# Optimization experiments

Measured on AMD Instinct MI355X. Metric: run time of the kernel, lower is better.

## Reference

```python
import jax, jax.numpy as jnp
import numpy as np

N = 6144          # active voxels / points
C = 96            # embed_channels
B = 2             # batch size
D = H = W = 32    # sparse spatial shape
K = 16            # PFAS kNN
DEPTH = 4
GRID_OPTS = np.array([[0.1, 0.1, 0.1], [0.4, 0.4, 0.4], [0.2, 0.2, 0.2]], dtype=np.float32)
BN_EPS = 1e-5


def _bn(x, g, b):
    # BatchNorm1d in training mode: batch stats over the point dim, biased var
    m = x.mean(0)
    v = jnp.var(x, axis=0)
    return (x - m) * jax.lax.rsqrt(v + BN_EPS) * g + b


def _seg_sum(x, seg):
    return jax.ops.segment_sum(x, seg, num_segments=N)


def _forward(indices, x, fp_w, fp_b, fp_g, fp_be, att_w1, att_b1, att_w2, att_b2,
             ff_w1, ff_b1, ff_g, ff_be, ff_w2, ff_b2, sa_w1, sa_b1, sa_w2, sa_b2,
             fj_w1, fj_b1, fj_g, fj_be, fj_w2, fj_b2,
             proj_w, proj_g, proj_be, lw_w, lw_g, lw_be, w_w, adp_w,
             fuse_w, fuse_g, fuse_be, conv1_w, bn1_g, bn1_be, conv2_w, bn2_g, bn2_be):
    # ---- CMPFE ----
    p = jax.nn.relu(_bn(x @ fp_w.T + fp_b, fp_g, fp_be))            # [N,9]
    cd, cl, nm = p[:, :3], p[:, 3:6], p[:, 6:9]

    def _att(f, i):
        h = jax.nn.relu(f @ att_w1[i].T + att_b1[i])
        return jax.nn.sigmoid(h @ att_w2[i].T + att_b2[i])

    enh = jnp.concatenate([cd, cl * _att(cl, 0), nm * _att(nm, 1)], axis=1)
    fu = jax.nn.relu(_bn(enh @ ff_w1.T + ff_b1, ff_g, ff_be)) @ ff_w2.T + ff_b2
    sem = jax.nn.sigmoid(jax.nn.relu(fu @ sa_w1.T + sa_b1) @ sa_w2.T + sa_b2)
    feat = fu * sem + x * (1.0 - sem)                               # new x.features

    # ---- PFAS: kNN geometry stats ----
    coord = indices[:, 1:].astype(jnp.float32)                      # [N,3]
    batch = indices[:, 0]
    sq = jnp.sum(coord * coord, axis=1)
    d2 = sq[:, None] + sq[None, :] - 2.0 * (coord @ coord.T)
    dist = jnp.sqrt(jnp.maximum(d2, 1e-12))
    same = batch[None, :] == batch[:, None]
    eye = jnp.eye(N, dtype=bool)
    dist = jnp.where(same & ~eye, dist, jnp.inf)
    neg_nd, idx = jax.lax.top_k(-dist, K)                           # K nearest
    nbr = coord[idx]                                                # [N,K,3]
    cent = nbr - nbr.mean(axis=1, keepdims=True)
    cov = jnp.einsum('nkd,nke->nde', cent, cent) / (K - 1)
    S = jnp.linalg.svd(cov, compute_uv=False)                       # [N,3] descending
    Sn = S / (S.sum(axis=1, keepdims=True) + 1e-6)
    linearity = Sn[:, 0:1] - (Sn[:, 1] + Sn[:, 2])[:, None]
    mean_dist = (-neg_nd).mean(axis=1, keepdims=True)
    density = 1.0 / (mean_dist + 1e-6)
    fl = jax.nn.relu(_bn(feat @ fj_w1.T + fj_b1, fj_g, fj_be)) @ fj_w2.T + fj_b2
    fp_ = jax.nn.softmax(fl, axis=1)
    tower = (density * 2.0 + fp_[:, 0:1]) / 3.0
    backg = (jnp.maximum(1.0 - linearity, 1.0 - density) + fp_[:, 1:2]) / 3.0
    line = (linearity * 2.0 + fp_[:, 2:3]) / 3.0
    go = jnp.asarray(GRID_OPTS)
    lg = go[2] * jnp.array([1.0, 1.0, 5.0], jnp.float32)            # last dim *5
    grid_sizes = tower * go[0] + backg * go[1] + line * lg + 1e-6   # [N,3]

    # ---- representative grids (N > 200 path) ----
    gm = grid_sizes.mean(axis=1)
    order = jnp.argsort(gm)
    reps = [grid_sizes[order[100:200]].mean(0),
            grid_sizes[order[::-1][:100]].mean(0),
            grid_sizes[order[:100]].mean(0)]

    # ---- voxel-grid clustering (torch_geometric voxel_grid + unique inverse) ----
    start = coord.min(axis=0)

    def _cluster(size):
        size = jnp.clip(size, 1e-6, None)
        c = jnp.clip(jnp.floor((coord - start) / size).astype(jnp.int64), 0, 4095)
        mx = c.max(axis=0) + 1
        ids = ((batch.astype(jnp.int64) * mx[0] + c[:, 0]) * mx[1] + c[:, 1]) * mx[2] + c[:, 2]
        _, inv = jnp.unique(ids, return_inverse=True, size=N, fill_value=0)
        return inv.reshape(-1)

    # ---- adaptive multi-branch scatter softmax aggregation ----
    branch_feats = []
    for i in range(DEPTH - 1):
        seg = _cluster(reps[i])
        cnt = jnp.maximum(_seg_sum(jnp.ones((N, 1), feat.dtype), seg), 1.0)
        pw = jax.nn.relu(_bn(feat @ lw_w[i].T, lw_g[i], lw_be[i]))
        pw = pw - (_seg_sum(pw, seg) / cnt)[seg]
        pw = pw @ w_w[i].T
        pw = jnp.exp(pw - pw.max())
        pw = pw / (_seg_sum(pw, seg)[seg] + 1e-6)
        pf = jax.nn.relu(_bn(feat @ proj_w[i].T, proj_g[i], proj_be[i])) * pw
        branch_feats.append(_seg_sum(pf, seg)[seg])
    adp = jax.nn.softmax(feat @ adp_w.T, axis=1)                    # [N,3]
    agg = jnp.einsum('nc,ncd->nd', adp, jnp.stack(branch_feats, 1))
    last = jax.nn.relu(_bn(feat @ proj_w[-1].T, proj_g[-1], proj_be[-1]))
    fused = jax.nn.relu(_bn(jnp.concatenate([last, agg], 1) @ fuse_w.T, fuse_g, fuse_be)) + feat
    res = fused

    # ---- submanifold sparse conv block (dense scatter form; inactive sites zero,
    #      outputs gathered only at active sites == SubMConv3d) ----
    bi, zi, yi, xi = indices[:, 0], indices[:, 1], indices[:, 2], indices[:, 3]

    def _subm(f, w):
        grid = jnp.zeros((B, D, H, W, C), f.dtype).at[bi, zi, yi, xi].set(f)
        o = jax.lax.conv_general_dilated(grid, w, (1, 1, 1), 'SAME',
                                         dimension_numbers=('NDHWC', 'DHWIO', 'NDHWC'))
        return o[bi, zi, yi, xi]

    f1 = jax.nn.relu(_bn(_subm(fused, conv1_w), bn1_g, bn1_be))
    f2 = _bn(_subm(f1, conv2_w), bn2_g, bn2_be)
    return jax.nn.relu(f2 + res)


def setup_inputs() -> dict:
    key = jax.random.key(0)
    ks = iter(jax.random.split(key, 64))

    def rn(*shape, s=0.05):
        return jax.random.normal(next(ks), shape, jnp.float32) * s

    # unique active voxel coordinates
    rng = np.random.default_rng(0)
    flat = rng.choice(B * D * H * W, size=N, replace=False)
    b = flat // (D * H * W)
    r = flat % (D * H * W)
    z = r // (H * W)
    y = (r % (H * W)) // W
    xw = r % W
    indices = jnp.asarray(np.stack([b, z, y, xw], 1).astype(np.int32))
    Ch = C // 2
    return {
        'x': jax.random.normal(next(ks), (N, C), jnp.float32),
        'indices': indices,
        'fp_w': rn(9, C), 'fp_b': rn(9), 'fp_g': jnp.ones(9), 'fp_be': jnp.zeros(9),
        'att_w1': rn(2, 16, 3), 'att_b1': rn(2, 16), 'att_w2': rn(2, 3, 16), 'att_b2': rn(2, 3),
        'ff_w1': rn(C, 9), 'ff_b1': rn(C), 'ff_g': jnp.ones(C), 'ff_be': jnp.zeros(C),
        'ff_w2': rn(C, C), 'ff_b2': rn(C),
        'sa_w1': rn(Ch, C), 'sa_b1': rn(Ch), 'sa_w2': rn(1, Ch), 'sa_b2': rn(1),
        'fj_w1': rn(64, C), 'fj_b1': rn(64), 'fj_g': jnp.ones(64), 'fj_be': jnp.zeros(64),
        'fj_w2': rn(3, 64), 'fj_b2': rn(3),
        'proj_w': rn(DEPTH, C, C), 'proj_g': jnp.ones((DEPTH, C)), 'proj_be': jnp.zeros((DEPTH, C)),
        'lw_w': rn(DEPTH - 1, C, C), 'lw_g': jnp.ones((DEPTH - 1, C)), 'lw_be': jnp.zeros((DEPTH - 1, C)),
        'w_w': rn(DEPTH - 1, C, C),
        'adp_w': rn(DEPTH - 1, C),
        'fuse_w': rn(C, 2 * C), 'fuse_g': jnp.ones(C), 'fuse_be': jnp.zeros(C),
        'conv1_w': rn(3, 3, 3, C, C), 'bn1_g': jnp.ones(C), 'bn1_be': jnp.zeros(C),
        'conv2_w': rn(3, 3, 3, C, C), 'bn2_g': jnp.ones(C), 'bn2_be': jnp.zeros(C),
    }


def reference(x, indices, fp_w, fp_b, fp_g, fp_be, att_w1, att_b1, att_w2, att_b2,
              ff_w1, ff_b1, ff_g, ff_be, ff_w2, ff_b2, sa_w1, sa_b1, sa_w2, sa_b2,
              fj_w1, fj_b1, fj_g, fj_be, fj_w2, fj_b2,
              proj_w, proj_g, proj_be, lw_w, lw_g, lw_be, w_w, adp_w,
              fuse_w, fuse_g, fuse_be, conv1_w, bn1_g, bn1_be, conv2_w, bn2_g, bn2_be):
    return _forward(indices, x, fp_w, fp_b, fp_g, fp_be, att_w1, att_b1, att_w2, att_b2,
                    ff_w1, ff_b1, ff_g, ff_be, ff_w2, ff_b2, sa_w1, sa_b1, sa_w2, sa_b2,
                    fj_w1, fj_b1, fj_g, fj_be, fj_w2, fj_b2,
                    proj_w, proj_g, proj_be, lw_w, lw_g, lw_be, w_w, adp_w,
                    fuse_w, fuse_g, fuse_be, conv1_w, bn1_g, bn1_be, conv2_w, bn2_g, bn2_be)
```

## Files before the change

kernel.cpp:

```cpp
#include <hip/hip_runtime.h>
#include <cstdint>

#define NPTS 6144
#define CH 96
#define NCELEM (NPTS*CH)
#define HTSZ 16384

__device__ __forceinline__ unsigned fenc(float f){
  unsigned u = __float_as_uint(f);
  return (u & 0x80000000u) ? ~u : (u | 0x80000000u);
}
__device__ __forceinline__ float fdec(unsigned u){
  unsigned b = (u & 0x80000000u) ? (u & 0x7FFFFFFFu) : ~u;
  return __uint_as_float(b);
}

__device__ void eig3(double a00,double a01,double a02,double a11,double a12,double a22,
                     double &e0,double &e1,double &e2){
  double p1 = a01*a01 + a02*a02 + a12*a12;
  double q = (a00+a11+a22)/3.0;
  double b00=a00-q, b11=a11-q, b22=a22-q;
  double p2 = b00*b00 + b11*b11 + b22*b22 + 2.0*p1;
  if (p2 <= 1e-300){ e0=e1=e2=q; return; }
  double pp = sqrt(p2/6.0);
  double inv = 1.0/pp;
  double c00=b00*inv, c01=a01*inv, c02=a02*inv, c11=b11*inv, c12=a12*inv, c22=b22*inv;
  double det = c00*(c11*c22-c12*c12) - c01*(c01*c22-c12*c02) + c02*(c01*c12-c11*c02);
  double r = det*0.5;
  r = r < -1.0 ? -1.0 : (r > 1.0 ? 1.0 : r);
  double phi = acos(r)/3.0;
  e0 = q + 2.0*pp*cos(phi);
  e2 = q + 2.0*pp*cos(phi + 2.0943951023931953);
  e1 = 3.0*q - e0 - e2;
}

__global__ void k_zero(int* p, long n){
  long i = (long)blockIdx.x*blockDim.x + threadIdx.x;
  long st = (long)gridDim.x*blockDim.x;
  for (; i < n; i += st) p[i] = 0;
}
__global__ void k_init(int* table, int* startmin){
  int i = blockIdx.x*blockDim.x + threadIdx.x;
  if (i < 2*32*32*32) table[i] = -1;
  if (i < 3) startmin[i] = 0x7fffffff;
}
__global__ void k_htinit(unsigned long long* keys, int* vals){
  int i = blockIdx.x*blockDim.x + threadIdx.x;
  if (i < 3*HTSZ){ keys[i] = ~0ull; vals[i] = 0x7fffffff; }
}
__global__ void k_pack_min(const int* __restrict__ ind, unsigned* __restrict__ packed, int* startmin){
  __shared__ int mn[3];
  if (threadIdx.x < 3) mn[threadIdx.x] = 0x7fffffff;
  __syncthreads();
  int p = blockIdx.x*blockDim.x + threadIdx.x;
  if (p < NPTS){
    int b = ind[p*4], z = ind[p*4+1], y = ind[p*4+2], x = ind[p*4+3];
    packed[p] = (unsigned)((b<<15)|(z<<10)|(y<<5)|x);
    atomicMin(&mn[0], z); atomicMin(&mn[1], y); atomicMin(&mn[2], x);
  }
  __syncthreads();
  if (threadIdx.x < 3) atomicMin(&startmin[threadIdx.x], mn[threadIdx.x]);
}

__global__ void __launch_bounds__(256) k_mm(
    const float* __restrict__ Abase, const float* __restrict__ Wbase,
    const float* __restrict__ biasBase, float* __restrict__ Obase,
    int CIN, int COUT,
    long sA, long sW, long sO, long sBias,
    const float* __restrict__ statsBase, long sStats,
    const float* __restrict__ gBase, const float* __restrict__ beBase, long sGB,
    const float* __restrict__ SsumBase, const int* __restrict__ segBase, const int* __restrict__ cntBase,
    unsigned* maxenc, int mode)
{
  int zb = blockIdx.y;
  const float* A = Abase + (long)zb*sA;
  const float* W = Wbase + (long)zb*sW;
  float* O = Obase + (long)zb*sO;
  const float* st = statsBase ? statsBase + (long)zb*sStats : nullptr;
  const float* g  = gBase ? gBase + (long)zb*sGB : nullptr;
  const float* be = beBase ? beBase + (long)zb*sGB : nullptr;
  const float* Ss = SsumBase ? SsumBase + (long)zb*NCELEM : nullptr;
  const int* seg  = segBase ? segBase + (long)zb*NPTS : nullptr;
  const int* cnt  = cntBase ? cntBase + (long)zb*NPTS : nullptr;

  __shared__ float Al[32*97];
  __shared__ float Wl[96*97];
  int tid = threadIdx.x;
  int r0 = blockIdx.x*32;
  for (int idx = tid; idx < CIN*COUT; idx += 256){
    int co = idx / CIN, k = idx - co*CIN;
    Wl[k*97 + co] = W[idx];
  }
  for (int idx = tid; idx < 32*CIN; idx += 256){
    int ir = idx / CIN, k = idx - ir*CIN;
    int row = r0 + ir;
    float v = A[(long)row*CIN + k];
    if (mode >= 1) v = fmaxf((v - st[k*2])*st[k*2+1]*g[k] + be[k], 0.f);
    if (mode == 2){
      int s = seg[row];
      float cf = fmaxf((float)cnt[s], 1.f);
      v -= Ss[(long)s*CH + k] / cf;
    }
    Al[ir*97 + k] = v;
  }
  __syncthreads();
  float lmax = -3.4e38f;
  if (COUT == 96){
    int rp = tid >> 4, cg = tid & 15;
    int co0 = cg*6;
    float acc0[6], acc1[6];
    #pragma unroll
    for (int j=0;j<6;++j){
      float b = biasBase ? biasBase[(long)zb*sBias + co0 + j] : 0.f;
      acc0[j] = b; acc1[j] = b;
    }
    int ra = 2*rp, rb = ra+1;
    for (int k=0;k<CIN;++k){
      float a0 = Al[ra*97+k], a1 = Al[rb*97+k];
      #pragma unroll
      for (int j=0;j<6;++j){
        float w = Wl[k*97+co0+j];
        acc0[j] = fmaf(a0, w, acc0[j]);
        acc1[j] = fmaf(a1, w, acc1[j]);
      }
    }
    #pragma unroll
    for (int j=0;j<6;++j){
      O[(long)(r0+ra)*96 + co0 + j] = acc0[j];
      O[(long)(r0+rb)*96 + co0 + j] = acc1[j];
      lmax = fmaxf(lmax, fmaxf(acc0[j], acc1[j]));
    }
  } else {
    for (int idx = tid; idx < 32*COUT; idx += 256){
      int ir = idx/COUT, co = idx - ir*COUT;
      float acc = biasBase ? biasBase[(long)zb*sBias + co] : 0.f;
      for (int k=0;k<CIN;++k) acc = fmaf(Al[ir*97+k], Wl[k*97+co], acc);
      O[(long)(r0+ir)*COUT + co] = acc;
      lmax = fmaxf(lmax, acc);
    }
  }
  if (maxenc){
    __shared__ float rmx[256];
    rmx[tid] = lmax; __syncthreads();
    for (int s2=128; s2>0; s2>>=1){
      if (tid < s2) rmx[tid] = fmaxf(rmx[tid], rmx[tid+s2]);
      __syncthreads();
    }
    if (tid == 0) atomicMax(&maxenc[zb], fenc(rmx[0]));
  }
}

__global__ void __launch_bounds__(256) k_mm_fuse(
    const float* __restrict__ tp3, const float* __restrict__ st,
    const float* __restrict__ pg3, const float* __restrict__ pbe3,
    const float* __restrict__ agg, const float* __restrict__ fw, float* __restrict__ tf)
{
  __shared__ float Al[32*193];
  __shared__ float Wl[96*97];
  int tid = threadIdx.x, r0 = blockIdx.x*32;
  for (int idx = tid; idx < 32*192; idx += 256){
    int ir = idx/192, k = idx - ir*192;
    int row = r0 + ir;
    float v;
    if (k < 96){
      v = tp3[(long)row*96 + k];
      v = fmaxf((v - st[k*2])*st[k*2+1]*pg3[k] + pbe3[k], 0.f);
    } else {
      v = agg[(long)row*96 + (k-96)];
    }
    Al[ir*193 + k] = v;
  }
  int rp = tid >> 4, cg = tid & 15, co0 = cg*6;
  float acc0[6] = {0,0,0,0,0,0}, acc1[6] = {0,0,0,0,0,0};
  int ra = 2*rp, rb = ra+1;
  for (int h=0; h<2; ++h){
    __syncthreads();
    for (int idx = tid; idx < 96*96; idx += 256){
      int co = idx/96, k = idx - co*96;
      Wl[k*97+co] = fw[(long)co*192 + h*96 + k];
    }
    __syncthreads();
    for (int k=0;k<96;++k){
      float a0 = Al[ra*193 + h*96 + k], a1 = Al[rb*193 + h*96 + k];
      #pragma unroll
      for (int j=0;j<6;++j){
        float w = Wl[k*97+co0+j];
        acc0[j] = fmaf(a0, w, acc0[j]);
        acc1[j] = fmaf(a1, w, acc1[j]);
      }
    }
  }
  #pragma unroll
  for (int j=0;j<6;++j){
    tf[(long)(r0+ra)*96 + co0 + j] = acc0[j];
    tf[(long)(r0+rb)*96 + co0 + j] = acc1[j];
  }
}

__global__ void k_stats(const float* __restrict__ Abase, long sA, int COLS,
                        float* __restrict__ statsBase, long sStats){
  int col = blockIdx.x, zb = blockIdx.y;
  const float* A = Abase + (long)zb*sA;
  double s = 0.0, q = 0.0;
  for (int r = threadIdx.x; r < NPTS; r += 256){
    double v = (double)A[(long)r*COLS + col];
    s += v; q += v*v;
  }
  __shared__ double ls[256], lq[256];
  ls[threadIdx.x] = s; lq[threadIdx.x] = q; __syncthreads();
  for (int t=128; t>0; t>>=1){
    if (threadIdx.x < t){ ls[threadIdx.x] += ls[threadIdx.x+t]; lq[threadIdx.x] += lq[threadIdx.x+t]; }
    __syncthreads();
  }
  if (threadIdx.x == 0){
    double mean = ls[0]/NPTS;
    double var = lq[0]/NPTS - mean*mean;
    float* stp = statsBase + (long)zb*sStats + col*2;
    stp[0] = (float)mean;
    stp[1] = (float)(1.0/sqrt(var + 1e-5));
  }
}

__global__ void k_p_att_enh(const float* __restrict__ t9, const float* __restrict__ st,
                            const float* __restrict__ fg, const float* __restrict__ fbe,
                            const float* __restrict__ aw1, const float* __restrict__ ab1,
                            const float* __restrict__ aw2, const float* __restrict__ ab2,
                            float* __restrict__ enh){
  int p = blockIdx.x*blockDim.x + threadIdx.x;
  if (p >= NPTS) return;
  float pp[9];
  #pragma unroll
  for (int c=0;c<9;++c){
    float v = t9[p*9+c];
    pp[c] = fmaxf((v - st[c*2])*st[c*2+1]*fg[c] + fbe[c], 0.f);
  }
  float eo[9];
  eo[0]=pp[0]; eo[1]=pp[1]; eo[2]=pp[2];
  #pragma unroll
  for (int i=0;i<2;++i){
    const float* w1 = aw1 + i*48;
    const float* b1 = ab1 + i*16;
    const float* w2 = aw2 + i*48;
    const float* b2 = ab2 + i*3;
    const float* f = pp + 3 + i*3;
    float h[16];
    #pragma unroll
    for (int j=0;j<16;++j){
      float s = b1[j];
      #pragma unroll
      for (int k=0;k<3;++k) s = fmaf(f[k], w1[j*3+k], s);
      h[j] = fmaxf(s, 0.f);
    }
    #pragma unroll
    for (int o=0;o<3;++o){
      float s = b2[o];
      #pragma unroll
      for (int j=0;j<16;++j) s = fmaf(h[j], w2[o*16+j], s);
      float a = 1.f/(1.f + expf(-s));
      eo[3+i*3+o] = f[o]*a;
    }
  }
  #pragma unroll
  for (int c=0;c<9;++c) enh[p*9+c] = eo[c];
}

__global__ void __launch_bounds__(256) k_sem_feat(
    const float* __restrict__ fu, const float* __restrict__ x,
    const float* __restrict__ w1, const float* __restrict__ b1,
    const float* __restrict__ w2, const float* __restrict__ b2,
    float* __restrict__ feat){
  int wid = (blockIdx.x*blockDim.x + threadIdx.x) >> 6;
  int lane = threadIdx.x & 63;
  if (wid >= NPTS) return;
  const float* fr = fu + (long)wid*96;
  float partial = 0.f;
  if (lane < 48){
    float h = b1[lane];
    for (int k=0;k<96;++k) h = fmaf(fr[k], w1[lane*96+k], h);
    h = fmaxf(h, 0.f);
    partial = h * w2[lane];
  }
  for (int m=32; m; m>>=1) partial += __shfl_xor(partial, m);
  float sem = 1.f/(1.f + expf(-(partial + b2[0])));
  for (int c=lane; c<96; c+=64){
    float f = fr[c];
    feat[(long)wid*96+c] = f*sem + x[(long)wid*96+c]*(1.f - sem);
  }
}

__global__ void __launch_bounds__(256) k_knn(const unsigned* __restrict__ packed,
                                             float* __restrict__ density, float* __restrict__ linearity){
  __shared__ unsigned pk[NPTS];
  for (int i=threadIdx.x; i<NPTS; i+=256) pk[i] = packed[i];
  __syncthreads();
  int pid = blockIdx.x*4 + (threadIdx.x>>6);
  int lane = threadIdx.x & 63;
  unsigned mypc = pk[pid];
  int myb = (int)(mypc>>15);
  int mz = (int)((mypc>>10)&31), my_=(int)((mypc>>5)&31), mx_=(int)(mypc&31);
  const unsigned T = 36u;
  int cnt = 0;
  for (int it=0; it<96; ++it){
    int j = lane + it*64;
    unsigned pc = pk[j];
    int dz = (int)((pc>>10)&31) - mz;
    int dy = (int)((pc>>5)&31) - my_;
    int dx = (int)(pc&31) - mx_;
    unsigned d2 = (unsigned)(dz*dz + dy*dy + dx*dx);
    cnt += (j != pid && (int)(pc>>15) == myb && d2 <= T) ? 1 : 0;
  }
  for (int m=32; m; m>>=1) cnt += __shfl_xor(cnt, m);
  unsigned lim = (cnt >= 16) ? T : 0xFFFFFFFFu;
  unsigned s[16];
  #pragma unroll
  for (int t=0;t<16;++t) s[t] = 0xFFFFFFFFu;
  for (int it=0; it<96; ++it){
    int j = lane + it*64;
    unsigned pc = pk[j];
    if (j != pid && (int)(pc>>15) == myb){
      int dz = (int)((pc>>10)&31) - mz;
      int dy = (int)((pc>>5)&31) - my_;
      int dx = (int)(pc&31) - mx_;
      unsigned d2 = (unsigned)(dz*dz + dy*dy + dx*dx);
      if (d2 <= lim){
        unsigned key = (d2<<13) | (unsigned)j;
        if (key < s[15]){
          s[15] = key;
          #pragma unroll
          for (int t=15;t>0;--t){
            unsigned a = s[t-1], b = s[t];
            unsigned lo = a<b?a:b, hi = a<b?b:a;
            s[t-1]=lo; s[t]=hi;
          }
        }
      }
    }
  }
  float sdist = 0.f;
  int sz=0,sy=0,sx=0,szz=0,syy=0,sxx=0,szy=0,szx=0,syx=0;
  for (int r=0;r<16;++r){
    unsigned m = s[0];
    #pragma unroll
    for (int w=32; w; w>>=1){
      unsigned o = (unsigned)__shfl_xor((int)m, w);
      m = m<o ? m : o;
    }
    bool own = (s[0] == m);
    #pragma unroll
    for (int t=0;t<15;++t) s[t] = own ? s[t+1] : s[t];
    if (own) s[15] = 0xFFFFFFFFu;
    unsigned idx = m & 8191u;
    unsigned d2 = m >> 13;
    sdist += sqrtf((float)d2);
    unsigned pc = pk[idx];
    int nz=(int)((pc>>10)&31), ny=(int)((pc>>5)&31), nx=(int)(pc&31);
    sz+=nz; sy+=ny; sx+=nx;
    szz+=nz*nz; syy+=ny*ny; sxx+=nx*nx; szy+=nz*ny; szx+=nz*nx; syx+=ny*nx;
  }
  if (lane == 0){
    double m0 = sz/16.0, m1 = sy/16.0, m2 = sx/16.0;
    float c00 = (float)(((double)szz - 16.0*m0*m0)/15.0);
    float c11 = (float)(((double)syy - 16.0*m1*m1)/15.0);
    float c22 = (float)(((double)sxx - 16.0*m2*m2)/15.0);
    float c01 = (float)(((double)szy - 16.0*m0*m1)/15.0);
    float c02 = (float)(((double)szx - 16.0*m0*m2)/15.0);
    float c12 = (float)(((double)syx - 16.0*m1*m2)/15.0);
    double e0,e1,e2;
    eig3((double)c00,(double)c01,(double)c02,(double)c11,(double)c12,(double)c22, e0,e1,e2);
    float s0 = (float)fabs(e0), s1 = (float)fabs(e1), s2 = (float)fabs(e2);
    float den = s0 + s1 + s2 + 1e-6f;
    float sn0 = s0/den, sn1 = s1/den, sn2 = s2/den;
    linearity[pid] = sn0 - (sn1 + sn2);
    float md = sdist * (1.f/16.f);
    density[pid] = 1.f/(md + 1e-6f);
  }
}

__global__ void k_geo(const float* __restrict__ t64, const float* __restrict__ st,
                      const float* __restrict__ fg, const float* __restrict__ fbe,
                      const float* __restrict__ w2, const float* __restrict__ b2,
                      const float* __restrict__ density, const float* __restrict__ linearity,
                      float* __restrict__ gsz, float* __restrict__ gm){
  int p = blockIdx.x*blockDim.x + threadIdx.x;
  if (p >= NPTS) return;
  float fl[3];
  #pragma unroll
  for (int o=0;o<3;++o) fl[o] = b2[o];
  for (int k=0;k<64;++k){
    float v = t64[(long)p*64+k];
    v = fmaxf((v - st[k*2])*st[k*2+1]*fg[k] + fbe[k], 0.f);
    #pragma unroll
    for (int o=0;o<3;++o) fl[o] = fmaf(v, w2[o*64+k], fl[o]);
  }
  float mx = fmaxf(fl[0], fmaxf(fl[1], fl[2]));
  float e0 = expf(fl[0]-mx), e1 = expf(fl[1]-mx), e2 = expf(fl[2]-mx);
  float es = e0+e1+e2;
  float p0 = e0/es, p1 = e1/es, p2 = e2/es;
  float den = density[p], lin = linearity[p];
  float tw = (den*2.f + p0)/3.f;
  float bg = (fmaxf(1.f-lin, 1.f-den) + p1)/3.f;
  float ln = (lin*2.f + p2)/3.f;
  float g0 = tw*0.1f + bg*0.4f + ln*0.2f + 1e-6f;
  float g1 = tw*0.1f + bg*0.4f + ln*0.2f + 1e-6f;
  float g2 = tw*0.1f + bg*0.4f + ln*1.0f + 1e-6f;
  gsz[p*3+0]=g0; gsz[p*3+1]=g1; gsz[p*3+2]=g2;
  gm[p] = (g0+g1+g2)/3.f;
}

#define RNKCHUNK 768
__global__ void __launch_bounds__(256) k_rank(const float* __restrict__ gm, int* __restrict__ rank){
  __shared__ unsigned long long lk[RNKCHUNK];
  int j0 = blockIdx.y*RNKCHUNK;
  for (int i=threadIdx.x; i<RNKCHUNK; i+=256){
    int j = j0 + i;
    lk[i] = (((unsigned long long)fenc(gm[j]))<<13) | (unsigned long long)j;
  }
  __syncthreads();
  int p = blockIdx.x*256 + threadIdx.x;
  unsigned long long myk = (((unsigned long long)fenc(gm[p]))<<13) | (unsigned long long)p;
  int cnt = 0;
  #pragma unroll 4
  for (int i=0; i<RNKCHUNK; ++i) cnt += (lk[i] < myk) ? 1 : 0;
  atomicAdd(&rank[p], cnt);
}
__global__ void k_scatter(const int* __restrict__ rank, const float* __restrict__ gsz,
                          float* __restrict__ bkt){
  int p = blockIdx.x*blockDim.x + threadIdx.x;
  if (p >= NPTS) return;
  int r = rank[p];
  int z = -1, t = 0;
  if (r < 100){ z = 2; t = r; }
  else if (r < 200){ z = 0; t = r - 100; }
  else if (r >= NPTS-100){ z = 1; t = r - (NPTS-100); }
  if (z >= 0){
    #pragma unroll
    for (int d=0; d<3; ++d) bkt[(z*100 + t)*3 + d] = gsz[p*3+d];
  }
}
__global__ void k_reps(const float* __restrict__ bkt, float* __restrict__ reps){
  int i = threadIdx.x;
  if (i >= 9) return;
  int z = i/3, d = i - z*3;
  double s = 0.0;
  for (int t=0; t<100; ++t) s += (double)bkt[(z*100 + t)*3 + d];
  reps[i] = (float)(s/100.0);
}

__global__ void k_cluster_c(const int* __restrict__ ind, const float* __restrict__ reps,
                            const int* __restrict__ startmin, int* __restrict__ cbuf, int* mxbuf){
  int z = blockIdx.y;
  int p = blockIdx.x*blockDim.x + threadIdx.x;
  __shared__ int lmx[3];
  if (threadIdx.x < 3) lmx[threadIdx.x] = 0;
  __syncthreads();
  if (p < NPTS){
    #pragma unroll
    for (int d=0; d<3; ++d){
      float sizev = fmaxf(reps[z*3+d], 1e-6f);
      float cf = floorf(((float)ind[p*4+1+d] - (float)startmin[d]) / sizev);
      int ci = (int)cf;
      ci = ci < 0 ? 0 : (ci > 4095 ? 4095 : ci);
      cbuf[((long)z*NPTS + p)*3 + d] = ci;
      atomicMax(&lmx[d], ci);
    }
  }
  __syncthreads();
  if (threadIdx.x < 3) atomicMax(&mxbuf[z*3+threadIdx.x], lmx[threadIdx.x]);
}
__global__ void k_cluster_ids(const int* __restrict__ ind, const int* __restrict__ cbuf,
                              const int* __restrict__ mxbuf, long long* __restrict__ ids){
  int z = blockIdx.y;
  int p = blockIdx.x*blockDim.x + threadIdx.x;
  if (p >= NPTS) return;
  long long mx0 = mxbuf[z*3+0]+1, mx1 = mxbuf[z*3+1]+1, mx2 = mxbuf[z*3+2]+1;
  long long b = ind[p*4];
  const int* cc = cbuf + ((long)z*NPTS + p)*3;
  ids[(long)z*NPTS + p] = ((b*mx0 + cc[0])*mx1 + cc[1])*mx2 + cc[2];
}

__device__ __forceinline__ int ht_hash(unsigned long long id){
  unsigned long long h = id * 0x9E3779B97F4A7C15ull;
  return (int)(h >> 49) & (HTSZ-1);
}
__global__ void k_seg_build(const long long* __restrict__ ids,
                            unsigned long long* __restrict__ keys, int* __restrict__ vals){
  int z = blockIdx.y;
  int p = blockIdx.x*blockDim.x + threadIdx.x;
  if (p >= NPTS) return;
  unsigned long long id = (unsigned long long)ids[(long)z*NPTS + p];
  unsigned long long* K = keys + (long)z*HTSZ;
  int* V = vals + (long)z*HTSZ;
  int slot = ht_hash(id);
  while (true){
    unsigned long long prev = atomicCAS(&K[slot], ~0ull, id);
    if (prev == ~0ull || prev == id){ atomicMin(&V[slot], p); break; }
    slot = (slot + 1) & (HTSZ-1);
  }
}
__global__ void k_seg_lookup(const long long* __restrict__ ids,
                             const unsigned long long* __restrict__ keys, const int* __restrict__ vals,
                             int* __restrict__ seg, int* __restrict__ cnt){
  int z = blockIdx.y;
  int p = blockIdx.x*blockDim.x + threadIdx.x;
  if (p >= NPTS) return;
  unsigned long long id = (unsigned long long)ids[(long)z*NPTS + p];
  const unsigned long long* K = keys + (long)z*HTSZ;
  int slot = ht_hash(id);
  while (K[slot] != id) slot = (slot + 1) & (HTSZ-1);
  int rep = vals[(long)z*HTSZ + slot];
  seg[(long)z*NPTS + p] = rep;
  atomicAdd(&cnt[(long)z*NPTS + rep], 1);
}

__global__ void k_pw_accum(const float* __restrict__ tlw, const float* __restrict__ stats,
                           const float* __restrict__ g, const float* __restrict__ be,
                           const int* __restrict__ seg, float* __restrict__ S){
  int z = blockIdx.y;
  int idx = blockIdx.x*blockDim.x + threadIdx.x;
  int p = idx/CH, c = idx - p*CH;
  const float* st = stats + z*192;
  float v = tlw[(long)z*NCELEM + idx];
  v = fmaxf((v - st[c*2])*st[c*2+1]*g[z*CH+c] + be[z*CH+c], 0.f);
  atomicAdd(&S[(long)z*NCELEM + (long)seg[(long)z*NPTS+p]*CH + c], v);
}
__global__ void k_exp_accum(const float* __restrict__ pw2, const unsigned* __restrict__ maxenc,
                            const int* __restrict__ seg, float* __restrict__ E){
  int z = blockIdx.y;
  int idx = blockIdx.x*blockDim.x + threadIdx.x;
  int p = idx/CH, c = idx - p*CH;
  float mv = fdec(maxenc[z]);
  float v = expf(pw2[(long)z*NCELEM + idx] - mv);
  atomicAdd(&E[(long)z*NCELEM + (long)seg[(long)z*NPTS+p]*CH + c], v);
}
__global__ void k_pf_accum(const float* __restrict__ tp, const float* __restrict__ stats,
                           const float* __restrict__ pg, const float* __restrict__ pbe,
                           const float* __restrict__ pw2, const unsigned* __restrict__ maxenc,
                           const int* __restrict__ seg, const float* __restrict__ E,
                           float* __restrict__ F){
  int z = blockIdx.y;
  int idx = blockIdx.x*blockDim.x + threadIdx.x;
  int p = idx/CH, c = idx - p*CH;
  const float* st = stats + z*192;
  float v = tp[(long)z*NCELEM + idx];
  v = fmaxf((v - st[c*2])*st[c*2+1]*pg[z*CH+c] + pbe[z*CH+c], 0.f);
  float mv = fdec(maxenc[z]);
  int sg = seg[(long)z*NPTS+p];
  float w = expf(pw2[(long)z*NCELEM + idx] - mv) / (E[(long)z*NCELEM + (long)sg*CH + c] + 1e-6f);
  atomicAdd(&F[(long)z*NCELEM + (long)sg*CH + c], v*w);
}
__global__ void k_adp(const float* __restrict__ feat, const float* __restrict__ aw,
                      float* __restrict__ adp){
  int p = blockIdx.x*blockDim.x + threadIdx.x;
  if (p >= NPTS) return;
  float a0=0.f, a1=0.f, a2=0.f;
  for (int k=0;k<CH;++k){
    float f = feat[(long)p*CH+k];
    a0 = fmaf(f, aw[k], a0);
    a1 = fmaf(f, aw[CH+k], a1);
    a2 = fmaf(f, aw[2*CH+k], a2);
  }
  float m = fmaxf(a0, fmaxf(a1,a2));
  float e0 = expf(a0-m), e1 = expf(a1-m), e2 = expf(a2-m);
  float s = e0+e1+e2;
  adp[p*3]=e0/s; adp[p*3+1]=e1/s; adp[p*3+2]=e2/s;
}
__global__ void k_agg(const float* __restrict__ adp, const float* __restrict__ F,
                      const int* __restrict__ seg, float* __restrict__ agg){
  int idx = blockIdx.x*blockDim.x + threadIdx.x;
  int p = idx/CH, c = idx - p*CH;
  float s = 0.f;
  #pragma unroll
  for (int z=0;z<3;++z)
    s = fmaf(adp[p*3+z], F[(long)z*NCELEM + (long)seg[(long)z*NPTS+p]*CH + c], s);
  agg[idx] = s;
}

__global__ void k_fused(const float* __restrict__ tf, const float* __restrict__ st,
                        const float* __restrict__ fg, const float* __restrict__ fbe,
                        const float* __restrict__ feat, float* __restrict__ fused){
  int idx = blockIdx.x*blockDim.x + threadIdx.x;
  int c = idx % CH;
  float v = tf[idx];
  v = fmaxf((v - st[c*2])*st[c*2+1]*fg[c] + fbe[c], 0.f);
  fused[idx] = v + feat[idx];
}
__global__ void k_table(const int* __restrict__ ind, int* __restrict__ table){
  int p = blockIdx.x*blockDim.x + threadIdx.x;
  if (p >= NPTS) return;
  int b = ind[p*4], z = ind[p*4+1], y = ind[p*4+2], x = ind[p*4+3];
  table[((b*32+z)*32+y)*32+x] = p;
}
__global__ void k_nbr(const int* __restrict__ ind, const int* __restrict__ table,
                      int* __restrict__ nbrtab){
  int idx = blockIdx.x*blockDim.x + threadIdx.x;
  if (idx >= NPTS*27) return;
  int p = idx/27, tap = idx - p*27;
  int dz = tap/9 - 1;
  int rm = tap % 9;
  int dy = rm/3 - 1, dx = rm%3 - 1;
  int b = ind[p*4], z = ind[p*4+1]+dz, y = ind[p*4+2]+dy, x = ind[p*4+3]+dx;
  int q = -1;
  if ((unsigned)z < 32u && (unsigned)y < 32u && (unsigned)x < 32u)
    q = table[((b*32+z)*32+y)*32+x];
  nbrtab[idx] = q;
}
__global__ void __launch_bounds__(256) k_convlist(const int* __restrict__ nbrtab,
                                                  int* __restrict__ tapcnt,
                                                  int* __restrict__ ptlist){
  __shared__ int lcnt[27], lbase[27], lpos[27];
  int tid = threadIdx.x;
  if (tid < 27){ lcnt[tid] = 0; lpos[tid] = 0; }
  __syncthreads();
  int base = blockIdx.x * 6912;
  for (int i = tid; i < 6912; i += 256){
    int idx = base + i;
    if (nbrtab[idx] >= 0) atomicAdd(&lcnt[idx % 27], 1);
  }
  __syncthreads();
  if (tid < 27) lbase[tid] = atomicAdd(&tapcnt[tid], lcnt[tid]);
  __syncthreads();
  for (int i = tid; i < 6912; i += 256){
    int idx = base + i;
    int q = nbrtab[idx];
    if (q >= 0){
      int tap = idx % 27;
      int p = idx / 27;
      int pos = lbase[tap] + atomicAdd(&lpos[tap], 1);
      ptlist[tap*NPTS + pos] = (p<<16) | q;
    }
  }
}
__global__ void __launch_bounds__(256) k_conv_gemm(
    const float* __restrict__ src, const float* __restrict__ Wc,
    const int* __restrict__ tapcnt, const int* __restrict__ ptlist,
    float* __restrict__ out){
  int tap = blockIdx.y;
  int n = tapcnt[tap];
  int r0 = blockIdx.x*32;
  if (r0 >= n) return;
  __shared__ float Al[32*97];
  __shared__ float Wl[96*97];
  __shared__ int pqs[32];
  int tid = threadIdx.x;
  if (tid < 32){
    int r = r0 + tid;
    pqs[tid] = (r < n) ? ptlist[tap*NPTS + r] : -1;
  }
  __syncthreads();
  for (int idx4 = tid; idx4 < 2304; idx4 += 256){
    int ci = idx4/24, c4 = idx4 - ci*24;
    float4 w = ((const float4*)(Wc + ((long)tap*96 + ci)*96))[c4];
    float* d = &Wl[ci*97 + c4*4];
    d[0]=w.x; d[1]=w.y; d[2]=w.z; d[3]=w.w;
  }
  for (int idx4 = tid; idx4 < 32*24; idx4 += 256){
    int ir = idx4/24, c4 = idx4 - ir*24;
    int pq = pqs[ir];
    float4 s = make_float4(0.f,0.f,0.f,0.f);
    if (pq >= 0){
      int q = pq & 0xFFFF;
      s = ((const float4*)(src + (long)q*CH))[c4];
    }
    float* d = &Al[ir*97 + c4*4];
    d[0]=s.x; d[1]=s.y; d[2]=s.z; d[3]=s.w;
  }
  __syncthreads();
  int rp = tid >> 4, cg = tid & 15;
  int co0 = cg*6;
  int ra = 2*rp, rb = ra+1;
  float acc0[6]={0,0,0,0,0,0}, acc1[6]={0,0,0,0,0,0};
  for (int k=0;k<96;++k){
    float a0 = Al[ra*97+k], a1 = Al[rb*97+k];
    #pragma unroll
    for (int j=0;j<6;++j){
      float w = Wl[k*97+co0+j];
      acc0[j] = fmaf(a0, w, acc0[j]);
      acc1[j] = fmaf(a1, w, acc1[j]);
    }
  }
  int pa = pqs[ra], pb = pqs[rb];
  if (pa >= 0){
    float* o = out + (long)(pa>>16)*CH + co0;
    #pragma unroll
    for (int j=0;j<6;++j) atomicAdd(&o[j], acc0[j]);
  }
  if (pb >= 0){
    float* o = out + (long)(pb>>16)*CH + co0;
    #pragma unroll
    for (int j=0;j<6;++j) atomicAdd(&o[j], acc1[j]);
  }
}
__global__ void k_bnrelu(const float* __restrict__ a, const float* __restrict__ st,
                         const float* __restrict__ g, const float* __restrict__ be,
                         float* __restrict__ o){
  int idx = blockIdx.x*blockDim.x + threadIdx.x;
  int c = idx % CH;
  float v = a[idx];
  o[idx] = fmaxf((v - st[c*2])*st[c*2+1]*g[c] + be[c], 0.f);
}
__global__ void k_final(const float* __restrict__ c2, const float* __restrict__ st,
                        const float* __restrict__ g, const float* __restrict__ be,
                        const float* __restrict__ fused, float* __restrict__ out){
  int idx = blockIdx.x*blockDim.x + threadIdx.x;
  int c = idx % CH;
  float v = c2[idx];
  v = (v - st[c*2])*st[c*2+1]*g[c] + be[c];
  out[idx] = fmaxf(v + fused[idx], 0.f);
}

extern "C" void kernel_launch(void* const* d_in, const int* in_sizes, int n_in,
                              void* d_out, int out_size, void* d_ws, size_t ws_size,
                              hipStream_t stream)
{
  const float* x      = (const float*)d_in[0];
  const int*   ind    = (const int*)  d_in[1];
  const float* fp_w   = (const float*)d_in[2];
  const float* fp_b   = (const float*)d_in[3];
  const float* fp_g   = (const float*)d_in[4];
  const float* fp_be  = (const float*)d_in[5];
  const float* att_w1 = (const float*)d_in[6];
  const float* att_b1 = (const float*)d_in[7];
  const float* att_w2 = (const float*)d_in[8];
  const float* att_b2 = (const float*)d_in[9];
  const float* ff_w1  = (const float*)d_in[10];
  const float* ff_b1  = (const float*)d_in[11];
  const float* ff_g   = (const float*)d_in[12];
  const float* ff_be  = (const float*)d_in[13];
  const float* ff_w2  = (const float*)d_in[14];
  const float* ff_b2  = (const float*)d_in[15];
  const float* sa_w1  = (const float*)d_in[16];
  const float* sa_b1  = (const float*)d_in[17];
  const float* sa_w2  = (const float*)d_in[18];
  const float* sa_b2  = (const float*)d_in[19];
  const float* fj_w1  = (const float*)d_in[20];
  const float* fj_b1  = (const float*)d_in[21];
  const float* fj_g   = (const float*)d_in[22];
  const float* fj_be  = (const float*)d_in[23];
  const float* fj_w2  = (const float*)d_in[24];
  const float* fj_b2  = (const float*)d_in[25];
  const float* proj_w = (const float*)d_in[26];
  const float* proj_g = (const float*)d_in[27];
  const float* proj_be= (const float*)d_in[28];
  const float* lw_w   = (const float*)d_in[29];
  const float* lw_g   = (const float*)d_in[30];
  const float* lw_be  = (const float*)d_in[31];
  const float* w_w    = (const float*)d_in[32];
  const float* adp_w  = (const float*)d_in[33];
  const float* fuse_w = (const float*)d_in[34];
  const float* fuse_g = (const float*)d_in[35];
  const float* fuse_be= (const float*)d_in[36];
  const float* conv1_w= (const float*)d_in[37];
  const float* bn1_g  = (const float*)d_in[38];
  const float* bn1_be = (const float*)d_in[39];
  const float* conv2_w= (const float*)d_in[40];
  const float* bn2_g  = (const float*)d_in[41];
  const float* bn2_be = (const float*)d_in[42];
  float* outp = (float*)d_out;
  (void)in_sizes; (void)n_in; (void)out_size; (void)ws_size;

  char* ws = (char*)d_ws;
  size_t off = 0;
  auto alloc = [&](size_t bytes)->size_t{
    off = (off + 255) & ~(size_t)255;
    size_t o = off; off += bytes; return o;
  };
  const size_t FNC = (size_t)NCELEM*4;
  size_t o_packed = alloc((size_t)NPTS*4);
  size_t o_start  = alloc(16);
  size_t o_dens   = alloc((size_t)NPTS*4);
  size_t o_lin    = alloc((size_t)NPTS*4);
  size_t o_t9     = alloc((size_t)NPTS*9*4);
  size_t o_enh    = alloc((size_t)NPTS*9*4);
  size_t o_gm     = alloc((size_t)NPTS*4);
  size_t o_gsz    = alloc((size_t)NPTS*3*4);
  size_t o_reps   = alloc(16*4);
  size_t o_bkt    = alloc((size_t)3*100*3*4);
  size_t o_cbuf   = alloc((size_t)3*NPTS*3*4);
  size_t o_ids    = alloc((size_t)3*NPTS*8);
  size_t o_seg    = alloc((size_t)3*NPTS*4);
  size_t o_adp    = alloc((size_t)NPTS*3*4);
  size_t o_table  = alloc((size_t)65536*4);
  size_t o_nbr    = alloc((size_t)NPTS*27*4);
  size_t o_ptlist = alloc((size_t)27*NPTS*4);
  size_t o_t64    = alloc((size_t)NPTS*64*4);
  size_t o_stats  = alloc((size_t)13*192*4);
  size_t o_htk    = alloc((size_t)3*HTSZ*8);
  size_t o_htv    = alloc((size_t)3*HTSZ*4);
  size_t o_S      = alloc(3*FNC);
  size_t o_E      = alloc(3*FNC);
  size_t o_F      = alloc(3*FNC);
  size_t o_c1     = alloc(FNC);
  size_t o_c2     = alloc(FNC);
  size_t o_cnt    = alloc((size_t)3*NPTS*4);
  size_t o_rank   = alloc((size_t)NPTS*4);
  size_t o_tapcnt = alloc(32*4);
  size_t o_mx     = alloc(16*4);
  size_t o_maxenc = alloc(16*4);
  size_t zend = off;
  size_t o_T96 = alloc(FNC);
  size_t o_fu  = alloc(FNC);
  size_t o_feat= alloc(FNC);
  size_t o_tlw = alloc(3*FNC);
  size_t o_pw2 = alloc(3*FNC);
  size_t o_tp  = alloc(4*FNC);
  size_t o_agg = alloc(FNC);
  size_t o_tf  = alloc(FNC);
  size_t o_fsd = alloc(FNC);
  size_t o_f1  = alloc(FNC);

  float* stats = (float*)(ws + o_stats);
  long zcount = (long)((zend - o_S)/4);

  k_zero<<<dim3(2048), dim3(256), 0, stream>>>((int*)(ws+o_S), zcount);
  k_init<<<dim3(256), dim3(256), 0, stream>>>((int*)(ws+o_table), (int*)(ws+o_start));
  k_htinit<<<dim3((3*HTSZ+255)/256), dim3(256), 0, stream>>>((unsigned long long*)(ws+o_htk), (int*)(ws+o_htv));
  k_pack_min<<<dim3(24), dim3(256), 0, stream>>>(ind, (unsigned*)(ws+o_packed), (int*)(ws+o_start));

  k_mm<<<dim3(192,1), 256, 0, stream>>>(x, fp_w, fp_b, (float*)(ws+o_t9), 96, 9,
      0,0,0,0, nullptr,0, nullptr,nullptr,0, nullptr,nullptr,nullptr, nullptr, 0);
  k_stats<<<dim3(9,1), 256, 0, stream>>>((float*)(ws+o_t9), 0, 9, stats+0*192, 0);
  k_p_att_enh<<<dim3(24), 256, 0, stream>>>((float*)(ws+o_t9), stats+0*192, fp_g, fp_be,
      att_w1, att_b1, att_w2, att_b2, (float*)(ws+o_enh));

  k_mm<<<dim3(192,1), 256, 0, stream>>>((float*)(ws+o_enh), ff_w1, ff_b1, (float*)(ws+o_T96), 9, 96,
      0,0,0,0, nullptr,0, nullptr,nullptr,0, nullptr,nullptr,nullptr, nullptr, 0);
  k_stats<<<dim3(96,1), 256, 0, stream>>>((float*)(ws+o_T96), 0, 96, stats+1*192, 0);
  k_mm<<<dim3(192,1), 256, 0, stream>>>((float*)(ws+o_T96), ff_w2, ff_b2, (float*)(ws+o_fu), 96, 96,
      0,0,0,0, stats+1*192,0, ff_g, ff_be,0, nullptr,nullptr,nullptr, nullptr, 1);

  k_sem_feat<<<dim3(1536), 256, 0, stream>>>((float*)(ws+o_fu), x, sa_w1, sa_b1, sa_w2, sa_b2,
      (float*)(ws+o_feat));

  k_knn<<<dim3(1536), 256, 0, stream>>>((unsigned*)(ws+o_packed), (float*)(ws+o_dens), (float*)(ws+o_lin));

  k_mm<<<dim3(192,1), 256, 0, stream>>>((float*)(ws+o_feat), fj_w1, fj_b1, (float*)(ws+o_t64), 96, 64,
      0,0,0,0, nullptr,0, nullptr,nullptr,0, nullptr,nullptr,nullptr, nullptr, 0);
  k_stats<<<dim3(64,1), 256, 0, stream>>>((float*)(ws+o_t64), 0, 64, stats+2*192, 0);
  k_geo<<<dim3(24), 256, 0, stream>>>((float*)(ws+o_t64), stats+2*192, fj_g, fj_be, fj_w2, fj_b2,
      (float*)(ws+o_dens), (float*)(ws+o_lin), (float*)(ws+o_gsz), (float*)(ws+o_gm));

  k_rank<<<dim3(24,8), 256, 0, stream>>>((float*)(ws+o_gm), (int*)(ws+o_rank));
  k_scatter<<<dim3(24), 256, 0, stream>>>((int*)(ws+o_rank), (float*)(ws+o_gsz), (float*)(ws+o_bkt));
  k_reps<<<dim3(1), 64, 0, stream>>>((float*)(ws+o_bkt), (float*)(ws+o_reps));

  k_cluster_c<<<dim3(24,3), 256, 0, stream>>>(ind, (float*)(ws+o_reps), (int*)(ws+o_start),
      (int*)(ws+o_cbuf), (int*)(ws+o_mx));
  k_cluster_ids<<<dim3(24,3), 256, 0, stream>>>(ind, (int*)(ws+o_cbuf), (int*)(ws+o_mx),
      (long long*)(ws+o_ids));
  k_seg_build<<<dim3(24,3), 256, 0, stream>>>((long long*)(ws+o_ids),
      (unsigned long long*)(ws+o_htk), (int*)(ws+o_htv));
  k_seg_lookup<<<dim3(24,3), 256, 0, stream>>>((long long*)(ws+o_ids),
      (unsigned long long*)(ws+o_htk), (int*)(ws+o_htv), (int*)(ws+o_seg), (int*)(ws+o_cnt));

  k_mm<<<dim3(192,3), 256, 0, stream>>>((float*)(ws+o_feat), lw_w, nullptr, (float*)(ws+o_tlw), 96, 96,
      0, 96*96, NCELEM, 0, nullptr,0, nullptr,nullptr,0, nullptr,nullptr,nullptr, nullptr, 0);
  k_stats<<<dim3(96,3), 256, 0, stream>>>((float*)(ws+o_tlw), NCELEM, 96, stats+3*192, 192);
  k_pw_accum<<<dim3(2304,3), 256, 0, stream>>>((float*)(ws+o_tlw), stats+3*192, lw_g, lw_be,
      (int*)(ws+o_seg), (float*)(ws+o_S));
  k_mm<<<dim3(192,3), 256, 0, stream>>>((float*)(ws+o_tlw), w_w, nullptr, (float*)(ws+o_pw2), 96, 96,
      NCELEM, 96*96, NCELEM, 0, stats+3*192,192, lw_g, lw_be,96,
      (float*)(ws+o_S), (int*)(ws+o_seg), (int*)(ws+o_cnt), (unsigned*)(ws+o_maxenc), 2);
  k_exp_accum<<<dim3(2304,3), 256, 0, stream>>>((float*)(ws+o_pw2), (unsigned*)(ws+o_maxenc),
      (int*)(ws+o_seg), (float*)(ws+o_E));
  k_mm<<<dim3(192,4), 256, 0, stream>>>((float*)(ws+o_feat), proj_w, nullptr, (float*)(ws+o_tp), 96, 96,
      0, 96*96, NCELEM, 0, nullptr,0, nullptr,nullptr,0, nullptr,nullptr,nullptr, nullptr, 0);
  k_stats<<<dim3(96,4), 256, 0, stream>>>((float*)(ws+o_tp), NCELEM, 96, stats+6*192, 192);
  k_pf_accum<<<dim3(2304,3), 256, 0, stream>>>((float*)(ws+o_tp), stats+6*192, proj_g, proj_be,
      (float*)(ws+o_pw2), (unsigned*)(ws+o_maxenc), (int*)(ws+o_seg), (float*)(ws+o_E), (float*)(ws+o_F));
  k_adp<<<dim3(24), 256, 0, stream>>>((float*)(ws+o_feat), adp_w, (float*)(ws+o_adp));
  k_agg<<<dim3(2304), 256, 0, stream>>>((float*)(ws+o_adp), (float*)(ws+o_F), (int*)(ws+o_seg),
      (float*)(ws+o_agg));

  k_mm_fuse<<<dim3(192), 256, 0, stream>>>((float*)(ws+o_tp) + (size_t)3*NCELEM, stats+9*192,
      proj_g + 3*96, proj_be + 3*96, (float*)(ws+o_agg), fuse_w, (float*)(ws+o_tf));
  k_stats<<<dim3(96,1), 256, 0, stream>>>((float*)(ws+o_tf), 0, 96, stats+10*192, 0);
  k_fused<<<dim3(2304), 256, 0, stream>>>((float*)(ws+o_tf), stats+10*192, fuse_g, fuse_be,
      (float*)(ws+o_feat), (float*)(ws+o_fsd));

  k_table<<<dim3(24), 256, 0, stream>>>(ind, (int*)(ws+o_table));
  k_nbr<<<dim3((NPTS*27+255)/256), 256, 0, stream>>>(ind, (int*)(ws+o_table), (int*)(ws+o_nbr));
  k_convlist<<<dim3(24), 256, 0, stream>>>((int*)(ws+o_nbr), (int*)(ws+o_tapcnt),
      (int*)(ws+o_ptlist));
  k_conv_gemm<<<dim3(192,27), 256, 0, stream>>>((float*)(ws+o_fsd), conv1_w,
      (int*)(ws+o_tapcnt), (int*)(ws+o_ptlist), (float*)(ws+o_c1));
  k_stats<<<dim3(96,1), 256, 0, stream>>>((float*)(ws+o_c1), 0, 96, stats+11*192, 0);
  k_bnrelu<<<dim3(2304), 256, 0, stream>>>((float*)(ws+o_c1), stats+11*192, bn1_g, bn1_be, (float*)(ws+o_f1));
  k_conv_gemm<<<dim3(192,27), 256, 0, stream>>>((float*)(ws+o_f1), conv2_w,
      (int*)(ws+o_tapcnt), (int*)(ws+o_ptlist), (float*)(ws+o_c2));
  k_stats<<<dim3(96,1), 256, 0, stream>>>((float*)(ws+o_c2), 0, 96, stats+12*192, 0);
  k_final<<<dim3(2304), 256, 0, stream>>>((float*)(ws+o_c2), stats+12*192, bn2_g, bn2_be,
      (float*)(ws+o_fsd), outp);
}
```

Measured before the change: 570.7 us.

## Replace brute-force kNN scan with dense voxel-table neighborhood lookup

New measurement: 543.9 us. -4.7%, faster.

```diff
diff --git a/kernel.cpp b/kernel.cpp
--- a/kernel.cpp
+++ b/kernel.cpp
@@ -289,6 +289,7 @@
 }
 
 __global__ void __launch_bounds__(256) k_knn(const unsigned* __restrict__ packed,
+                                             const int* __restrict__ table,
                                              float* __restrict__ density, float* __restrict__ linearity){
   __shared__ unsigned pk[NPTS];
   for (int i=threadIdx.x; i<NPTS; i+=256) pk[i] = packed[i];
@@ -298,31 +299,52 @@
   unsigned mypc = pk[pid];
   int myb = (int)(mypc>>15);
   int mz = (int)((mypc>>10)&31), my_=(int)((mypc>>5)&31), mx_=(int)(mypc&31);
-  const unsigned T = 36u;
-  int cnt = 0;
-  for (int it=0; it<96; ++it){
-    int j = lane + it*64;
-    unsigned pc = pk[j];
-    int dz = (int)((pc>>10)&31) - mz;
-    int dy = (int)((pc>>5)&31) - my_;
-    int dx = (int)(pc&31) - mx_;
-    unsigned d2 = (unsigned)(dz*dz + dy*dy + dx*dx);
-    cnt += (j != pid && (int)(pc>>15) == myb && d2 <= T) ? 1 : 0;
-  }
-  for (int m=32; m; m>>=1) cnt += __shfl_xor(cnt, m);
-  unsigned lim = (cnt >= 16) ? T : 0xFFFFFFFFu;
   unsigned s[16];
   #pragma unroll
   for (int t=0;t<16;++t) s[t] = 0xFFFFFFFFu;
-  for (int it=0; it<96; ++it){
-    int j = lane + it*64;
-    unsigned pc = pk[j];
-    if (j != pid && (int)(pc>>15) == myb){
-      int dz = (int)((pc>>10)&31) - mz;
-      int dy = (int)((pc>>5)&31) - my_;
-      int dx = (int)(pc&31) - mx_;
-      unsigned d2 = (unsigned)(dz*dz + dy*dy + dx*dx);
-      if (d2 <= lim){
+  int cnt = 0;
+  const int tbase = myb*32768;
+  for (int it=0; it<21; ++it){
+    int i = lane + it*64;
+    if (i < 1331){
+      int dz = i/121;
+      int rm = i - dz*121;
+      int dy = rm/11;
+      int dx = rm - dy*11;
+      dz -= 5; dy -= 5; dx -= 5;
+      int d2 = dz*dz + dy*dy + dx*dx;
+      int zz = mz+dz, yy = my_+dy, xx = mx_+dx;
+      if (d2 > 0 && d2 <= 25 &&
+          (unsigned)zz < 32u && (unsigned)yy < 32u && (unsigned)xx < 32u){
+        int j = table[tbase + (zz*32+yy)*32+xx];
+        if (j >= 0){
+          ++cnt;
+          unsigned key = ((unsigned)d2<<13) | (unsigned)j;
+          if (key < s[15]){
+            s[15] = key;
+            #pragma unroll
+            for (int t=15;t>0;--t){
+              unsigned a = s[t-1], b = s[t];
+              unsigned lo = a<b?a:b, hi = a<b?b:a;
+              s[t-1]=lo; s[t]=hi;
+            }
+          }
+        }
+      }
+    }
+  }
+  for (int m=32; m; m>>=1) cnt += __shfl_xor(cnt, m);
+  if (cnt < 16){
+    #pragma unroll
+    for (int t=0;t<16;++t) s[t] = 0xFFFFFFFFu;
+    for (int it=0; it<96; ++it){
+      int j = lane + it*64;
+      unsigned pc = pk[j];
+      if (j != pid && (int)(pc>>15) == myb){
+        int dz = (int)((pc>>10)&31) - mz;
+        int dy = (int)((pc>>5)&31) - my_;
+        int dx = (int)(pc&31) - mx_;
+        unsigned d2 = (unsigned)(dz*dz + dy*dy + dx*dx);
         unsigned key = (d2<<13) | (unsigned)j;
         if (key < s[15]){
           s[15] = key;
@@ -815,6 +837,7 @@
   k_init<<<dim3(256), dim3(256), 0, stream>>>((int*)(ws+o_table), (int*)(ws+o_start));
   k_htinit<<<dim3((3*HTSZ+255)/256), dim3(256), 0, stream>>>((unsigned long long*)(ws+o_htk), (int*)(ws+o_htv));
   k_pack_min<<<dim3(24), dim3(256), 0, stream>>>(ind, (unsigned*)(ws+o_packed), (int*)(ws+o_start));
+  k_table<<<dim3(24), 256, 0, stream>>>(ind, (int*)(ws+o_table));
 
   k_mm<<<dim3(192,1), 256, 0, stream>>>(x, fp_w, fp_b, (float*)(ws+o_t9), 96, 9,
       0,0,0,0, nullptr,0, nullptr,nullptr,0, nullptr,nullptr,nullptr, nullptr, 0);
@@ -831,7 +854,8 @@
   k_sem_feat<<<dim3(1536), 256, 0, stream>>>((float*)(ws+o_fu), x, sa_w1, sa_b1, sa_w2, sa_b2,
       (float*)(ws+o_feat));
 
-  k_knn<<<dim3(1536), 256, 0, stream>>>((unsigned*)(ws+o_packed), (float*)(ws+o_dens), (float*)(ws+o_lin));
+  k_knn<<<dim3(1536), 256, 0, stream>>>((unsigned*)(ws+o_packed), (int*)(ws+o_table),
+      (float*)(ws+o_dens), (float*)(ws+o_lin));
 
   k_mm<<<dim3(192,1), 256, 0, stream>>>((float*)(ws+o_feat), fj_w1, fj_b1, (float*)(ws+o_t64), 96, 64,
       0,0,0,0, nullptr,0, nullptr,nullptr,0, nullptr,nullptr,nullptr, nullptr, 0);
@@ -877,7 +901,6 @@
   k_fused<<<dim3(2304), 256, 0, stream>>>((float*)(ws+o_tf), stats+10*192, fuse_g, fuse_be,
       (float*)(ws+o_feat), (float*)(ws+o_fsd));
 
-  k_table<<<dim3(24), 256, 0, stream>>>(ind, (int*)(ws+o_table));
   k_nbr<<<dim3((NPTS*27+255)/256), 256, 0, stream>>>(ind, (int*)(ws+o_table), (int*)(ws+o_nbr));
   k_convlist<<<dim3(24), 256, 0, stream>>>((int*)(ws+o_nbr), (int*)(ws+o_tapcnt),
       (int*)(ws+o_ptlist));
```
